# Kernel optimization log

Measured on AMD Instinct MI355X. Metric: run time of the kernel, lower is better.

## Reference

```python
import jax, jax.numpy as jnp
import numpy as np

N = 50000   # nodes
E = 800000  # edges (avg degree 16)
IN = 128    # in_feats
D = 64      # h_feats
H = 4       # n_heads
NEG_SLOPE = 0.2  # DGL GATConv default leaky_relu slope
L = 3       # n_layers (conv_hs)


def setup_inputs() -> dict:
    key = jax.random.key(0)
    ks = jax.random.split(key, 16)
    s = 0.05
    inp = {
        "in_feat": jax.random.normal(ks[0], (N, IN), jnp.float32),
        "src": jax.random.randint(ks[1], (E,), 0, N),
        "dst": jax.random.randint(ks[2], (E,), 0, N),
        # conv1 params (DGL GATConv: fc no bias, attn_l/attn_r, output bias)
        "W1": jax.random.normal(ks[3], (IN, H * D), jnp.float32) * s,
        "al1": jax.random.normal(ks[4], (H, D), jnp.float32) * s,
        "ar1": jax.random.normal(ks[5], (H, D), jnp.float32) * s,
        "b1": jnp.zeros((H * D,), jnp.float32),
        # stacked hidden GATConv params (L layers)
        "Wh": jax.random.normal(ks[6], (L, D, H * D), jnp.float32) * s,
        "alh": jax.random.normal(ks[7], (L, H, D), jnp.float32) * s,
        "arh": jax.random.normal(ks[8], (L, H, D), jnp.float32) * s,
        "bh": jnp.zeros((L, H * D), jnp.float32),
        # out_ln: Linear(H*D -> D)
        "Wo": jax.random.normal(ks[9], (H * D, D), jnp.float32) * s,
        "bo": jnp.zeros((D,), jnp.float32),
    }
    return inp


def gat_conv(h, W, al, ar, b, src, dst):
    # h: [N, F_in] -> feat: [N, H, D]
    feat = (h @ W).reshape(N, H, -1)
    el = jnp.einsum('nhd,hd->nh', feat, al)  # [N, H]
    er = jnp.einsum('nhd,hd->nh', feat, ar)  # [N, H]
    e = jax.nn.leaky_relu(el[src] + er[dst], NEG_SLOPE)  # [E, H]
    # segment softmax over incoming edges of each dst node
    emax = jax.ops.segment_max(e, dst, num_segments=N)
    emax = jnp.where(jnp.isfinite(emax), emax, 0.0)  # guard empty segments
    a = jnp.exp(e - emax[dst])
    ssum = jax.ops.segment_sum(a, dst, num_segments=N)
    alpha = a / ssum[dst]  # [E, H]
    # weighted scatter-aggregate of source features
    out = jax.ops.segment_sum(feat[src] * alpha[:, :, None], dst, num_segments=N)
    return out + b.reshape(1, H, -1)  # [N, H, D]


def reference(in_feat, src, dst, W1, al1, ar1, b1, Wh, alh, arh, bh, Wo, bo):
    h = gat_conv(in_feat, W1, al1, ar1, b1, src, dst).mean(axis=1)  # [N, D]
    for i in range(L - 1):
        h = gat_conv(h, Wh[i], alh[i], arh[i], bh[i], src, dst).mean(axis=1)
    h = gat_conv(h, Wh[L - 1], alh[L - 1], arh[L - 1], bh[L - 1], src, dst)  # [N, H, D]
    h = h.reshape(N, H * D) @ Wo + bo  # [N, D]
    # LayerNorm(elementwise_affine=False)
    mu = h.mean(axis=-1, keepdims=True)
    var = ((h - mu) ** 2).mean(axis=-1, keepdims=True)
    return (h - mu) / jnp.sqrt(var + 1e-5)
```

## Files before the change

### kernel.cpp

```cpp
#include <hip/hip_runtime.h>

#define NN 50000
#define NE 800000

__device__ __forceinline__ float wsum64(float v) {
#pragma unroll
  for (int off = 32; off; off >>= 1) v += __shfl_xor(v, off, 64);
  return v;
}
__device__ __forceinline__ float lrelu(float x) { return x > 0.0f ? x : 0.2f * x; }

__global__ void zero_int_k(int* __restrict__ p, int n) {
  int i = blockIdx.x * 256 + threadIdx.x;
  if (i < n) p[i] = 0;
}

__global__ void count_deg_k(const int* __restrict__ dst, int* __restrict__ deg) {
  int e = blockIdx.x * 256 + threadIdx.x;
  if (e < NE) atomicAdd(&deg[dst[e]], 1);
}

__global__ __launch_bounds__(1024) void scan_k(const int* __restrict__ deg,
                                               int* __restrict__ row_ptr,
                                               int* __restrict__ cursor) {
  __shared__ int woff[16];
  int tid = threadIdx.x;
  int lane = tid & 63, wv = tid >> 6;
  const int CH = (NN + 1023) / 1024;
  int lo = tid * CH;
  int hi = lo + CH;
  if (lo > NN) lo = NN;
  if (hi > NN) hi = NN;
  int s = 0;
  for (int i = lo; i < hi; ++i) s += deg[i];
  int incl = s;
#pragma unroll
  for (int off = 1; off < 64; off <<= 1) {
    int t = __shfl_up(incl, off, 64);
    if (lane >= off) incl += t;
  }
  if (lane == 63) woff[wv] = incl;
  __syncthreads();
  if (tid == 0) {
    int run = 0;
#pragma unroll
    for (int w = 0; w < 16; ++w) { int t = woff[w]; woff[w] = run; run += t; }
    row_ptr[NN] = run;
  }
  __syncthreads();
  int run = incl - s + woff[wv];
  for (int i = lo; i < hi; ++i) {
    row_ptr[i] = run;
    cursor[i] = run;
    run += deg[i];
  }
}

__global__ void fill_csr_k(const int* __restrict__ src, const int* __restrict__ dst,
                           int* __restrict__ cursor, int* __restrict__ csr_src) {
  int e = blockIdx.x * 256 + threadIdx.x;
  if (e < NE) {
    int pos = atomicAdd(&cursor[dst[e]], 1);
    csr_src[pos] = src[e];
  }
}

__global__ void compute_q_k(const float* __restrict__ W, const float* __restrict__ al,
                            const float* __restrict__ ar, float* __restrict__ Q, int KDIM) {
  int idx = blockIdx.x * 256 + threadIdx.x;
  if (idx >= KDIM * 8) return;
  int k = idx >> 3, c = idx & 7;
  int h = c & 3;
  const float* av = (c < 4 ? al : ar) + h * 64;
  const float* wrow = W + (size_t)k * 256 + h * 64;
  float s = 0.0f;
  for (int m = 0; m < 64; ++m) s += wrow[m] * av[m];
  Q[idx] = s;
}

__global__ void compute_m_k(const float* __restrict__ Wh2, const float* __restrict__ Wo,
                            float* __restrict__ M) {
  int row = blockIdx.x;
  int d = threadIdx.x;
  int h = row >> 6, k = row & 63;
  float s = 0.0f;
  for (int j = 0; j < 64; ++j)
    s += Wh2[k * 256 + h * 64 + j] * Wo[(h * 64 + j) * 64 + d];
  M[row * 64 + d] = s;
}

__global__ void compute_c_k(const float* __restrict__ bh2, const float* __restrict__ Wo,
                            const float* __restrict__ bo, float* __restrict__ cvec) {
  int d = threadIdx.x;
  if (d >= 64) return;
  float s = bo[d];
  for (int m = 0; m < 256; ++m) s += bh2[m] * Wo[m * 64 + d];
  cvec[d] = s;
}

__global__ __launch_bounds__(256) void eler_l1_k(const float* __restrict__ X,
                                                 const float* __restrict__ Q,
                                                 float* __restrict__ elp,
                                                 float* __restrict__ erp) {
  int n = __builtin_amdgcn_readfirstlane(blockIdx.x * 4 + (threadIdx.x >> 6));
  int lane = threadIdx.x & 63;
  float2 xv = *(const float2*)&X[(n << 7) + (lane << 1)];
  float4 qa0 = *(const float4*)&Q[(lane * 2) * 8];
  float4 qb0 = *(const float4*)&Q[(lane * 2) * 8 + 4];
  float4 qa1 = *(const float4*)&Q[(lane * 2 + 1) * 8];
  float4 qb1 = *(const float4*)&Q[(lane * 2 + 1) * 8 + 4];
  float p[8];
  p[0] = xv.x * qa0.x + xv.y * qa1.x; p[1] = xv.x * qa0.y + xv.y * qa1.y;
  p[2] = xv.x * qa0.z + xv.y * qa1.z; p[3] = xv.x * qa0.w + xv.y * qa1.w;
  p[4] = xv.x * qb0.x + xv.y * qb1.x; p[5] = xv.x * qb0.y + xv.y * qb1.y;
  p[6] = xv.x * qb0.z + xv.y * qb1.z; p[7] = xv.x * qb0.w + xv.y * qb1.w;
#pragma unroll
  for (int c = 0; c < 8; ++c) p[c] = wsum64(p[c]);
  if (lane == 0) {
    *(float4*)&elp[n << 2] = make_float4(p[0], p[1], p[2], p[3]);
    *(float4*)&erp[n << 2] = make_float4(p[4], p[5], p[6], p[7]);
  }
}

__global__ __launch_bounds__(256) void fused_hidden_k(
    const float* __restrict__ x, const float* __restrict__ el,
    const float* __restrict__ er, const float* __restrict__ W,
    const float* __restrict__ b, const float* __restrict__ Qn,
    const int* __restrict__ row_ptr, const int* __restrict__ csr_src,
    float* __restrict__ hout, float* __restrict__ eln, float* __restrict__ ern) {
  __shared__ float gs[4 * 4 * 256];
  int wave = threadIdx.x >> 6, lane = threadIdx.x & 63;
  int q = lane >> 4, r = lane & 15;
  int base = (blockIdx.x * 4 + wave) * 4;
  float* gw = &gs[wave * 1024];
  int r4 = r << 2;
#pragma unroll 1
  for (int t = 0; t < 4; ++t) {
    int n = __builtin_amdgcn_readfirstlane(base + t);
    int beg = row_ptr[n], end = row_ptr[n + 1];
    float erq = er[(n << 2) + q];
    float4 a = make_float4(0.f, 0.f, 0.f, 0.f);
    float sw = 0.f;
#define ESTEP(elv, xv)                      \
  do {                                      \
    float w = __expf(lrelu((elv) + erq));   \
    sw += w;                                \
    a.x = fmaf(w, (xv).x, a.x);             \
    a.y = fmaf(w, (xv).y, a.y);             \
    a.z = fmaf(w, (xv).z, a.z);             \
    a.w = fmaf(w, (xv).w, a.w);             \
  } while (0)
    int j = beg;
    for (; j + 8 <= end; j += 8) {
      int s0 = csr_src[j + 0], s1 = csr_src[j + 1];
      int s2 = csr_src[j + 2], s3 = csr_src[j + 3];
      int s4 = csr_src[j + 4], s5 = csr_src[j + 5];
      int s6 = csr_src[j + 6], s7 = csr_src[j + 7];
      float e0 = el[(s0 << 2) + q], e1 = el[(s1 << 2) + q];
      float e2 = el[(s2 << 2) + q], e3 = el[(s3 << 2) + q];
      float e4 = el[(s4 << 2) + q], e5 = el[(s5 << 2) + q];
      float e6 = el[(s6 << 2) + q], e7 = el[(s7 << 2) + q];
      float4 x0 = *(const float4*)&x[(s0 << 6) + r4];
      float4 x1 = *(const float4*)&x[(s1 << 6) + r4];
      float4 x2 = *(const float4*)&x[(s2 << 6) + r4];
      float4 x3 = *(const float4*)&x[(s3 << 6) + r4];
      float4 x4 = *(const float4*)&x[(s4 << 6) + r4];
      float4 x5 = *(const float4*)&x[(s5 << 6) + r4];
      float4 x6 = *(const float4*)&x[(s6 << 6) + r4];
      float4 x7 = *(const float4*)&x[(s7 << 6) + r4];
      ESTEP(e0, x0); ESTEP(e1, x1); ESTEP(e2, x2); ESTEP(e3, x3);
      ESTEP(e4, x4); ESTEP(e5, x5); ESTEP(e6, x6); ESTEP(e7, x7);
    }
    for (; j < end; ++j) {
      int s0 = csr_src[j];
      float e0 = el[(s0 << 2) + q];
      float4 x0 = *(const float4*)&x[(s0 << 6) + r4];
      ESTEP(e0, x0);
    }
#undef ESTEP
    float inv = sw > 0.f ? 1.0f / sw : 0.f;
    *(float4*)&gw[t * 256 + (q << 6) + r4] =
        make_float4(a.x * inv, a.y * inv, a.z * inv, a.w * inv);
  }
  float y0 = 0.f, y1 = 0.f, y2 = 0.f, y3 = 0.f;
  for (int rr = 0; rr < 256; rr += 4) {
#pragma unroll
    for (int u = 0; u < 4; ++u) {
      int row = rr + u;
      int h = row >> 6, k = row & 63;
      float sv = W[k * 256 + (h << 6) + lane];
      y0 = fmaf(gw[0 * 256 + row], sv, y0);
      y1 = fmaf(gw[1 * 256 + row], sv, y1);
      y2 = fmaf(gw[2 * 256 + row], sv, y2);
      y3 = fmaf(gw[3 * 256 + row], sv, y3);
    }
  }
  float bsum = b[lane] + b[64 + lane] + b[128 + lane] + b[192 + lane];
  float4 qa = *(const float4*)&Qn[lane * 8];
  float4 qb = *(const float4*)&Qn[lane * 8 + 4];
  float ys[4] = {y0, y1, y2, y3};
#pragma unroll
  for (int t = 0; t < 4; ++t) {
    int n = base + t;
    float yv = 0.25f * (ys[t] + bsum);
    hout[(n << 6) + lane] = yv;
    float e0 = wsum64(yv * qa.x), e1 = wsum64(yv * qa.y);
    float e2 = wsum64(yv * qa.z), e3 = wsum64(yv * qa.w);
    float r0 = wsum64(yv * qb.x), r1 = wsum64(yv * qb.y);
    float r2 = wsum64(yv * qb.z), r3 = wsum64(yv * qb.w);
    if (lane == 0) {
      *(float4*)&eln[n << 2] = make_float4(e0, e1, e2, e3);
      *(float4*)&ern[n << 2] = make_float4(r0, r1, r2, r3);
    }
  }
}

__global__ __launch_bounds__(256) void fused_l1_k(
    const float* __restrict__ x, const float* __restrict__ el,
    const float* __restrict__ er, const float* __restrict__ W,
    const float* __restrict__ b, const float* __restrict__ Qn,
    const int* __restrict__ row_ptr, const int* __restrict__ csr_src,
    float* __restrict__ hout, float* __restrict__ eln, float* __restrict__ ern) {
  __shared__ float gs[4 * 4 * 512];
  int wave = threadIdx.x >> 6, lane = threadIdx.x & 63;
  int q = lane >> 4, r = lane & 15;
  int base = (blockIdx.x * 4 + wave) * 4;
  float* gw = &gs[wave * 2048];
  int r8 = r << 3;
#pragma unroll 1
  for (int t = 0; t < 4; ++t) {
    int n = __builtin_amdgcn_readfirstlane(base + t);
    int beg = row_ptr[n], end = row_ptr[n + 1];
    float erq = er[(n << 2) + q];
    float4 aA = make_float4(0.f, 0.f, 0.f, 0.f);
    float4 aB = make_float4(0.f, 0.f, 0.f, 0.f);
    float sw = 0.f;
#define ESTEP(elv, xa, xb)                  \
  do {                                      \
    float w = __expf(lrelu((elv) + erq));   \
    sw += w;                                \
    aA.x = fmaf(w, (xa).x, aA.x);           \
    aA.y = fmaf(w, (xa).y, aA.y);           \
    aA.z = fmaf(w, (xa).z, aA.z);           \
    aA.w = fmaf(w, (xa).w, aA.w);           \
    aB.x = fmaf(w, (xb).x, aB.x);           \
    aB.y = fmaf(w, (xb).y, aB.y);           \
    aB.z = fmaf(w, (xb).z, aB.z);           \
    aB.w = fmaf(w, (xb).w, aB.w);           \
  } while (0)
    int j = beg;
    for (; j + 4 <= end; j += 4) {
      int s0 = csr_src[j + 0], s1 = csr_src[j + 1];
      int s2 = csr_src[j + 2], s3 = csr_src[j + 3];
      float e0 = el[(s0 << 2) + q], e1 = el[(s1 << 2) + q];
      float e2 = el[(s2 << 2) + q], e3 = el[(s3 << 2) + q];
      float4 xa0 = *(const float4*)&x[(s0 << 7) + r8];
      float4 xb0 = *(const float4*)&x[(s0 << 7) + r8 + 4];
      float4 xa1 = *(const float4*)&x[(s1 << 7) + r8];
      float4 xb1 = *(const float4*)&x[(s1 << 7) + r8 + 4];
      float4 xa2 = *(const float4*)&x[(s2 << 7) + r8];
      float4 xb2 = *(const float4*)&x[(s2 << 7) + r8 + 4];
      float4 xa3 = *(const float4*)&x[(s3 << 7) + r8];
      float4 xb3 = *(const float4*)&x[(s3 << 7) + r8 + 4];
      ESTEP(e0, xa0, xb0); ESTEP(e1, xa1, xb1);
      ESTEP(e2, xa2, xb2); ESTEP(e3, xa3, xb3);
    }
    for (; j < end; ++j) {
      int s0 = csr_src[j];
      float e0 = el[(s0 << 2) + q];
      float4 xa0 = *(const float4*)&x[(s0 << 7) + r8];
      float4 xb0 = *(const float4*)&x[(s0 << 7) + r8 + 4];
      ESTEP(e0, xa0, xb0);
    }
#undef ESTEP
    float inv = sw > 0.f ? 1.0f / sw : 0.f;
    *(float4*)&gw[t * 512 + (q << 7) + r8] =
        make_float4(aA.x * inv, aA.y * inv, aA.z * inv, aA.w * inv);
    *(float4*)&gw[t * 512 + (q << 7) + r8 + 4] =
        make_float4(aB.x * inv, aB.y * inv, aB.z * inv, aB.w * inv);
  }
  float y0 = 0.f, y1 = 0.f, y2 = 0.f, y3 = 0.f;
  for (int rr = 0; rr < 512; rr += 4) {
#pragma unroll
    for (int u = 0; u < 4; ++u) {
      int row = rr + u;
      int h = row >> 7, k = row & 127;
      float sv = W[k * 256 + (h << 6) + lane];
      y0 = fmaf(gw[0 * 512 + row], sv, y0);
      y1 = fmaf(gw[1 * 512 + row], sv, y1);
      y2 = fmaf(gw[2 * 512 + row], sv, y2);
      y3 = fmaf(gw[3 * 512 + row], sv, y3);
    }
  }
  float bsum = b[lane] + b[64 + lane] + b[128 + lane] + b[192 + lane];
  float4 qa = *(const float4*)&Qn[lane * 8];
  float4 qb = *(const float4*)&Qn[lane * 8 + 4];
  float ys[4] = {y0, y1, y2, y3};
#pragma unroll
  for (int t = 0; t < 4; ++t) {
    int n = base + t;
    float yv = 0.25f * (ys[t] + bsum);
    hout[(n << 6) + lane] = yv;
    float e0 = wsum64(yv * qa.x), e1 = wsum64(yv * qa.y);
    float e2 = wsum64(yv * qa.z), e3 = wsum64(yv * qa.w);
    float r0 = wsum64(yv * qb.x), r1 = wsum64(yv * qb.y);
    float r2 = wsum64(yv * qb.z), r3 = wsum64(yv * qb.w);
    if (lane == 0) {
      *(float4*)&eln[n << 2] = make_float4(e0, e1, e2, e3);
      *(float4*)&ern[n << 2] = make_float4(r0, r1, r2, r3);
    }
  }
}

__global__ __launch_bounds__(256) void fused_final_k(
    const float* __restrict__ x, const float* __restrict__ el,
    const float* __restrict__ er, const float* __restrict__ M,
    const float* __restrict__ cvec, const int* __restrict__ row_ptr,
    const int* __restrict__ csr_src, float* __restrict__ out) {
  __shared__ float gs[4 * 4 * 256];
  int wave = threadIdx.x >> 6, lane = threadIdx.x & 63;
  int q = lane >> 4, r = lane & 15;
  int base = (blockIdx.x * 4 + wave) * 4;
  float* gw = &gs[wave * 1024];
  int r4 = r << 2;
#pragma unroll 1
  for (int t = 0; t < 4; ++t) {
    int n = __builtin_amdgcn_readfirstlane(base + t);
    int beg = row_ptr[n], end = row_ptr[n + 1];
    float erq = er[(n << 2) + q];
    float4 a = make_float4(0.f, 0.f, 0.f, 0.f);
    float sw = 0.f;
#define ESTEP(elv, xv)                      \
  do {                                      \
    float w = __expf(lrelu((elv) + erq));   \
    sw += w;                                \
    a.x = fmaf(w, (xv).x, a.x);             \
    a.y = fmaf(w, (xv).y, a.y);             \
    a.z = fmaf(w, (xv).z, a.z);             \
    a.w = fmaf(w, (xv).w, a.w);             \
  } while (0)
    int j = beg;
    for (; j + 8 <= end; j += 8) {
      int s0 = csr_src[j + 0], s1 = csr_src[j + 1];
      int s2 = csr_src[j + 2], s3 = csr_src[j + 3];
      int s4 = csr_src[j + 4], s5 = csr_src[j + 5];
      int s6 = csr_src[j + 6], s7 = csr_src[j + 7];
      float e0 = el[(s0 << 2) + q], e1 = el[(s1 << 2) + q];
      float e2 = el[(s2 << 2) + q], e3 = el[(s3 << 2) + q];
      float e4 = el[(s4 << 2) + q], e5 = el[(s5 << 2) + q];
      float e6 = el[(s6 << 2) + q], e7 = el[(s7 << 2) + q];
      float4 x0 = *(const float4*)&x[(s0 << 6) + r4];
      float4 x1 = *(const float4*)&x[(s1 << 6) + r4];
      float4 x2 = *(const float4*)&x[(s2 << 6) + r4];
      float4 x3 = *(const float4*)&x[(s3 << 6) + r4];
      float4 x4 = *(const float4*)&x[(s4 << 6) + r4];
      float4 x5 = *(const float4*)&x[(s5 << 6) + r4];
      float4 x6 = *(const float4*)&x[(s6 << 6) + r4];
      float4 x7 = *(const float4*)&x[(s7 << 6) + r4];
      ESTEP(e0, x0); ESTEP(e1, x1); ESTEP(e2, x2); ESTEP(e3, x3);
      ESTEP(e4, x4); ESTEP(e5, x5); ESTEP(e6, x6); ESTEP(e7, x7);
    }
    for (; j < end; ++j) {
      int s0 = csr_src[j];
      float e0 = el[(s0 << 2) + q];
      float4 x0 = *(const float4*)&x[(s0 << 6) + r4];
      ESTEP(e0, x0);
    }
#undef ESTEP
    float inv = sw > 0.f ? 1.0f / sw : 0.f;
    *(float4*)&gw[t * 256 + (q << 6) + r4] =
        make_float4(a.x * inv, a.y * inv, a.z * inv, a.w * inv);
  }
  float y0 = 0.f, y1 = 0.f, y2 = 0.f, y3 = 0.f;
  for (int rr = 0; rr < 256; rr += 4) {
#pragma unroll
    for (int u = 0; u < 4; ++u) {
      int row = rr + u;
      float sv = M[(row << 6) + lane];
      y0 = fmaf(gw[0 * 256 + row], sv, y0);
      y1 = fmaf(gw[1 * 256 + row], sv, y1);
      y2 = fmaf(gw[2 * 256 + row], sv, y2);
      y3 = fmaf(gw[3 * 256 + row], sv, y3);
    }
  }
  float cl = cvec[lane];
  float ys[4] = {y0 + cl, y1 + cl, y2 + cl, y3 + cl};
#pragma unroll
  for (int t = 0; t < 4; ++t) {
    int n = base + t;
    float y = ys[t];
    float mu = wsum64(y) * (1.0f / 64.0f);
    float dv = y - mu;
    float var = wsum64(dv * dv) * (1.0f / 64.0f);
    out[(n << 6) + lane] = dv * rsqrtf(var + 1e-5f);
  }
}

extern "C" void kernel_launch(void* const* d_in, const int* in_sizes, int n_in,
                              void* d_out, int out_size, void* d_ws, size_t ws_size,
                              hipStream_t stream) {
  const float* in_feat = (const float*)d_in[0];
  const int* src = (const int*)d_in[1];
  const int* dst = (const int*)d_in[2];
  const float* W1 = (const float*)d_in[3];
  const float* al1 = (const float*)d_in[4];
  const float* ar1 = (const float*)d_in[5];
  const float* b1 = (const float*)d_in[6];
  const float* Wh = (const float*)d_in[7];
  const float* alh = (const float*)d_in[8];
  const float* arh = (const float*)d_in[9];
  const float* bh = (const float*)d_in[10];
  const float* Wo = (const float*)d_in[11];
  const float* bo = (const float*)d_in[12];
  float* out = (float*)d_out;

  char* ws = (char*)d_ws;
  size_t off = 0;
  auto alloc = [&](size_t bytes) {
    void* p = ws + off;
    off = (off + bytes + 255) & ~(size_t)255;
    return p;
  };
  float* h_a = (float*)alloc((size_t)NN * 64 * 4);
  float* h_b = (float*)alloc((size_t)NN * 64 * 4);
  float* el_a = (float*)alloc((size_t)NN * 4 * 4);
  float* er_a = (float*)alloc((size_t)NN * 4 * 4);
  float* el_b = (float*)alloc((size_t)NN * 4 * 4);
  float* er_b = (float*)alloc((size_t)NN * 4 * 4);
  float* Q1 = (float*)alloc(128 * 8 * 4);
  float* Q2 = (float*)alloc(64 * 8 * 4);
  float* Q3 = (float*)alloc(64 * 8 * 4);
  float* Q4 = (float*)alloc(64 * 8 * 4);
  float* M = (float*)alloc(256 * 64 * 4);
  float* cvec = (float*)alloc(64 * 4);
  int* deg = (int*)alloc((size_t)NN * 4);
  int* row_ptr = (int*)alloc((size_t)(NN + 1) * 4);
  int* cursor = (int*)alloc((size_t)NN * 4);
  int* csr_src = (int*)alloc((size_t)NE * 4);
  (void)ws_size; (void)in_sizes; (void)n_in; (void)out_size;

  zero_int_k<<<(NN + 255) / 256, 256, 0, stream>>>(deg, NN);
  count_deg_k<<<(NE + 255) / 256, 256, 0, stream>>>(dst, deg);
  scan_k<<<1, 1024, 0, stream>>>(deg, row_ptr, cursor);
  fill_csr_k<<<(NE + 255) / 256, 256, 0, stream>>>(src, dst, cursor, csr_src);

  compute_q_k<<<4, 256, 0, stream>>>(W1, al1, ar1, Q1, 128);
  compute_q_k<<<2, 256, 0, stream>>>(Wh + 0 * 64 * 256, alh + 0 * 256, arh + 0 * 256, Q2, 64);
  compute_q_k<<<2, 256, 0, stream>>>(Wh + 1 * 64 * 256, alh + 1 * 256, arh + 1 * 256, Q3, 64);
  compute_q_k<<<2, 256, 0, stream>>>(Wh + 2 * 64 * 256, alh + 2 * 256, arh + 2 * 256, Q4, 64);
  compute_m_k<<<256, 64, 0, stream>>>(Wh + 2 * 64 * 256, Wo, M);
  compute_c_k<<<1, 64, 0, stream>>>(bh + 2 * 256, Wo, bo, cvec);

  const int FUSED_GRID = NN / 16;
  const int ELER_GRID = NN / 4;

  eler_l1_k<<<ELER_GRID, 256, 0, stream>>>(in_feat, Q1, el_a, er_a);
  fused_l1_k<<<FUSED_GRID, 256, 0, stream>>>(in_feat, el_a, er_a, W1, b1, Q2,
                                             row_ptr, csr_src, h_a, el_b, er_b);
  fused_hidden_k<<<FUSED_GRID, 256, 0, stream>>>(h_a, el_b, er_b, Wh + 0 * 64 * 256,
                                                 bh + 0 * 256, Q3, row_ptr, csr_src,
                                                 h_b, el_a, er_a);
  fused_hidden_k<<<FUSED_GRID, 256, 0, stream>>>(h_b, el_a, er_a, Wh + 1 * 64 * 256,
                                                 bh + 1 * 256, Q4, row_ptr, csr_src,
                                                 h_a, el_b, er_b);
  fused_final_k<<<FUSED_GRID, 256, 0, stream>>>(h_a, el_b, er_b, M, cvec,
                                                row_ptr, csr_src, out);
}
```

Baseline: 658.3 us.

## Bucket CSR edges by source-node slice to improve gather cache locality

```diff
diff --git a/kernel.cpp b/kernel.cpp
--- a/kernel.cpp
+++ b/kernel.cpp
@@ -2,6 +2,9 @@
 
 #define NN 50000
 #define NE 800000
+#define NB 4
+#define SLICE 12500
+#define NR2 (NN * NB)
 
 __device__ __forceinline__ float wsum64(float v) {
 #pragma unroll
@@ -9,30 +12,35 @@
   return v;
 }
 __device__ __forceinline__ float lrelu(float x) { return x > 0.0f ? x : 0.2f * x; }
+#define RFL(v) __builtin_amdgcn_readfirstlane(v)
 
 __global__ void zero_int_k(int* __restrict__ p, int n) {
   int i = blockIdx.x * 256 + threadIdx.x;
   if (i < n) p[i] = 0;
 }
 
-__global__ void count_deg_k(const int* __restrict__ dst, int* __restrict__ deg) {
+__global__ void count_deg2_k(const int* __restrict__ src, const int* __restrict__ dst,
+                             int* __restrict__ deg2) {
   int e = blockIdx.x * 256 + threadIdx.x;
-  if (e < NE) atomicAdd(&deg[dst[e]], 1);
-}
-
-__global__ __launch_bounds__(1024) void scan_k(const int* __restrict__ deg,
-                                               int* __restrict__ row_ptr,
-                                               int* __restrict__ cursor) {
+  if (e < NE) {
+    int b = src[e] / SLICE;
+    atomicAdd(&deg2[dst[e] * NB + b], 1);
+  }
+}
+
+__global__ __launch_bounds__(1024) void scan2_k(const int* __restrict__ deg2,
+                                                int* __restrict__ rp2,
+                                                int* __restrict__ cur2) {
   __shared__ int woff[16];
   int tid = threadIdx.x;
   int lane = tid & 63, wv = tid >> 6;
-  const int CH = (NN + 1023) / 1024;
+  const int CH = (NR2 + 1023) / 1024;
   int lo = tid * CH;
   int hi = lo + CH;
-  if (lo > NN) lo = NN;
-  if (hi > NN) hi = NN;
+  if (lo > NR2) lo = NR2;
+  if (hi > NR2) hi = NR2;
   int s = 0;
-  for (int i = lo; i < hi; ++i) s += deg[i];
+  for (int i = lo; i < hi; ++i) s += deg2[i];
   int incl = s;
 #pragma unroll
   for (int off = 1; off < 64; off <<= 1) {
@@ -45,23 +53,25 @@
     int run = 0;
 #pragma unroll
     for (int w = 0; w < 16; ++w) { int t = woff[w]; woff[w] = run; run += t; }
-    row_ptr[NN] = run;
+    rp2[NR2] = run;
   }
   __syncthreads();
   int run = incl - s + woff[wv];
   for (int i = lo; i < hi; ++i) {
-    row_ptr[i] = run;
-    cursor[i] = run;
-    run += deg[i];
-  }
-}
-
-__global__ void fill_csr_k(const int* __restrict__ src, const int* __restrict__ dst,
-                           int* __restrict__ cursor, int* __restrict__ csr_src) {
+    rp2[i] = run;
+    cur2[i] = run;
+    run += deg2[i];
+  }
+}
+
+__global__ void fill_csr2_k(const int* __restrict__ src, const int* __restrict__ dst,
+                            int* __restrict__ cur2, int* __restrict__ csr_src) {
   int e = blockIdx.x * 256 + threadIdx.x;
   if (e < NE) {
-    int pos = atomicAdd(&cursor[dst[e]], 1);
-    csr_src[pos] = src[e];
+    int sv = src[e];
+    int b = sv / SLICE;
+    int pos = atomicAdd(&cur2[dst[e] * NB + b], 1);
+    csr_src[pos] = sv;
   }
 }
 
@@ -102,7 +112,7 @@
                                                  const float* __restrict__ Q,
                                                  float* __restrict__ elp,
                                                  float* __restrict__ erp) {
-  int n = __builtin_amdgcn_readfirstlane(blockIdx.x * 4 + (threadIdx.x >> 6));
+  int n = RFL(blockIdx.x * 4 + (threadIdx.x >> 6));
   int lane = threadIdx.x & 63;
   float2 xv = *(const float2*)&X[(n << 7) + (lane << 1)];
   float4 qa0 = *(const float4*)&Q[(lane * 2) * 8];
@@ -122,65 +132,129 @@
   }
 }
 
+__device__ __forceinline__ void agg_bucket64(const float* __restrict__ x,
+                                             const float* __restrict__ el,
+                                             const int* __restrict__ csr,
+                                             int beg, int end, int q, int r4,
+                                             float erq, float4& a, float& sw) {
+  int j = beg;
+  for (; j + 4 <= end; j += 4) {
+    int s0 = csr[j + 0], s1 = csr[j + 1], s2 = csr[j + 2], s3 = csr[j + 3];
+    float e0 = el[(s0 << 2) + q], e1 = el[(s1 << 2) + q];
+    float e2 = el[(s2 << 2) + q], e3 = el[(s3 << 2) + q];
+    float4 x0 = *(const float4*)&x[(s0 << 6) + r4];
+    float4 x1 = *(const float4*)&x[(s1 << 6) + r4];
+    float4 x2 = *(const float4*)&x[(s2 << 6) + r4];
+    float4 x3 = *(const float4*)&x[(s3 << 6) + r4];
+    float w0 = __expf(lrelu(e0 + erq)), w1 = __expf(lrelu(e1 + erq));
+    float w2 = __expf(lrelu(e2 + erq)), w3 = __expf(lrelu(e3 + erq));
+    sw += w0 + w1 + w2 + w3;
+    a.x = fmaf(w0, x0.x, a.x); a.y = fmaf(w0, x0.y, a.y);
+    a.z = fmaf(w0, x0.z, a.z); a.w = fmaf(w0, x0.w, a.w);
+    a.x = fmaf(w1, x1.x, a.x); a.y = fmaf(w1, x1.y, a.y);
+    a.z = fmaf(w1, x1.z, a.z); a.w = fmaf(w1, x1.w, a.w);
+    a.x = fmaf(w2, x2.x, a.x); a.y = fmaf(w2, x2.y, a.y);
+    a.z = fmaf(w2, x2.z, a.z); a.w = fmaf(w2, x2.w, a.w);
+    a.x = fmaf(w3, x3.x, a.x); a.y = fmaf(w3, x3.y, a.y);
+    a.z = fmaf(w3, x3.z, a.z); a.w = fmaf(w3, x3.w, a.w);
+  }
+  for (; j < end; ++j) {
+    int s0 = csr[j];
+    float e0 = el[(s0 << 2) + q];
+    float4 x0 = *(const float4*)&x[(s0 << 6) + r4];
+    float w0 = __expf(lrelu(e0 + erq));
+    sw += w0;
+    a.x = fmaf(w0, x0.x, a.x); a.y = fmaf(w0, x0.y, a.y);
+    a.z = fmaf(w0, x0.z, a.z); a.w = fmaf(w0, x0.w, a.w);
+  }
+}
+
+__device__ __forceinline__ void agg_bucket128(const float* __restrict__ x,
+                                              const float* __restrict__ el,
+                                              const int* __restrict__ csr,
+                                              int beg, int end, int q, int r8,
+                                              float erq, float4& aA, float4& aB,
+                                              float& sw) {
+  int j = beg;
+  for (; j + 4 <= end; j += 4) {
+    int s0 = csr[j + 0], s1 = csr[j + 1], s2 = csr[j + 2], s3 = csr[j + 3];
+    float e0 = el[(s0 << 2) + q], e1 = el[(s1 << 2) + q];
+    float e2 = el[(s2 << 2) + q], e3 = el[(s3 << 2) + q];
+    float4 xa0 = *(const float4*)&x[(s0 << 7) + r8];
+    float4 xb0 = *(const float4*)&x[(s0 << 7) + r8 + 4];
+    float4 xa1 = *(const float4*)&x[(s1 << 7) + r8];
+    float4 xb1 = *(const float4*)&x[(s1 << 7) + r8 + 4];
+    float4 xa2 = *(const float4*)&x[(s2 << 7) + r8];
+    float4 xb2 = *(const float4*)&x[(s2 << 7) + r8 + 4];
+    float4 xa3 = *(const float4*)&x[(s3 << 7) + r8];
+    float4 xb3 = *(const float4*)&x[(s3 << 7) + r8 + 4];
+    float w0 = __expf(lrelu(e0 + erq)), w1 = __expf(lrelu(e1 + erq));
+    float w2 = __expf(lrelu(e2 + erq)), w3 = __expf(lrelu(e3 + erq));
+    sw += w0 + w1 + w2 + w3;
+    aA.x = fmaf(w0, xa0.x, aA.x); aA.y = fmaf(w0, xa0.y, aA.y);
+    aA.z = fmaf(w0, xa0.z, aA.z); aA.w = fmaf(w0, xa0.w, aA.w);
+    aB.x = fmaf(w0, xb0.x, aB.x); aB.y = fmaf(w0, xb0.y, aB.y);
+    aB.z = fmaf(w0, xb0.z, aB.z); aB.w = fmaf(w0, xb0.w, aB.w);
+    aA.x = fmaf(w1, xa1.x, aA.x); aA.y = fmaf(w1, xa1.y, aA.y);
+    aA.z = fmaf(w1, xa1.z, aA.z); aA.w = fmaf(w1, xa1.w, aA.w);
+    aB.x = fmaf(w1, xb1.x, aB.x); aB.y = fmaf(w1, xb1.y, aB.y);
+    aB.z = fmaf(w1, xb1.z, aB.z); aB.w = fmaf(w1, xb1.w, aB.w);
+    aA.x = fmaf(w2, xa2.x, aA.x); aA.y = fmaf(w2, xa2.y, aA.y);
+    aA.z = fmaf(w2, xa2.z, aA.z); aA.w = fmaf(w2, xa2.w, aA.w);
+    aB.x = fmaf(w2, xb2.x, aB.x); aB.y = fmaf(w2, xb2.y, aB.y);
+    aB.z = fmaf(w2, xb2.z, aB.z); aB.w = fmaf(w2, xb2.w, aB.w);
+    aA.x = fmaf(w3, xa3.x, aA.x); aA.y = fmaf(w3, xa3.y, aA.y);
+    aA.z = fmaf(w3, xa3.z, aA.z); aA.w = fmaf(w3, xa3.w, aA.w);
+    aB.x = fmaf(w3, xb3.x, aB.x); aB.y = fmaf(w3, xb3.y, aB.y);
+    aB.z = fmaf(w3, xb3.z, aB.z); aB.w = fmaf(w3, xb3.w, aB.w);
+  }
+  for (; j < end; ++j) {
+    int s0 = csr[j];
+    float e0 = el[(s0 << 2) + q];
+    float4 xa0 = *(const float4*)&x[(s0 << 7) + r8];
+    float4 xb0 = *(const float4*)&x[(s0 << 7) + r8 + 4];
+    float w0 = __expf(lrelu(e0 + erq));
+    sw += w0;
+    aA.x = fmaf(w0, xa0.x, aA.x); aA.y = fmaf(w0, xa0.y, aA.y);
+    aA.z = fmaf(w0, xa0.z, aA.z); aA.w = fmaf(w0, xa0.w, aA.w);
+    aB.x = fmaf(w0, xb0.x, aB.x); aB.y = fmaf(w0, xb0.y, aB.y);
+    aB.z = fmaf(w0, xb0.z, aB.z); aB.w = fmaf(w0, xb0.w, aB.w);
+  }
+}
+
 __global__ __launch_bounds__(256) void fused_hidden_k(
     const float* __restrict__ x, const float* __restrict__ el,
     const float* __restrict__ er, const float* __restrict__ W,
     const float* __restrict__ b, const float* __restrict__ Qn,
-    const int* __restrict__ row_ptr, const int* __restrict__ csr_src,
+    const int* __restrict__ rp2, const int* __restrict__ csr_src,
     float* __restrict__ hout, float* __restrict__ eln, float* __restrict__ ern) {
-  __shared__ float gs[4 * 4 * 256];
+  __shared__ float gs[4][1024];
   int wave = threadIdx.x >> 6, lane = threadIdx.x & 63;
-  int q = lane >> 4, r = lane & 15;
+  int q = lane >> 4, r = lane & 15, r4 = r << 2;
   int base = (blockIdx.x * 4 + wave) * 4;
-  float* gw = &gs[wave * 1024];
-  int r4 = r << 2;
+  float* gw = gs[wave];
+  float4 av[4];
+  float swv[4], erqv[4];
+#pragma unroll
+  for (int t = 0; t < 4; ++t) {
+    av[t] = make_float4(0.f, 0.f, 0.f, 0.f);
+    swv[t] = 0.f;
+    erqv[t] = er[((base + t) << 2) + q];
+  }
 #pragma unroll 1
-  for (int t = 0; t < 4; ++t) {
-    int n = __builtin_amdgcn_readfirstlane(base + t);
-    int beg = row_ptr[n], end = row_ptr[n + 1];
-    float erq = er[(n << 2) + q];
-    float4 a = make_float4(0.f, 0.f, 0.f, 0.f);
-    float sw = 0.f;
-#define ESTEP(elv, xv)                      \
-  do {                                      \
-    float w = __expf(lrelu((elv) + erq));   \
-    sw += w;                                \
-    a.x = fmaf(w, (xv).x, a.x);             \
-    a.y = fmaf(w, (xv).y, a.y);             \
-    a.z = fmaf(w, (xv).z, a.z);             \
-    a.w = fmaf(w, (xv).w, a.w);             \
-  } while (0)
-    int j = beg;
-    for (; j + 8 <= end; j += 8) {
-      int s0 = csr_src[j + 0], s1 = csr_src[j + 1];
-      int s2 = csr_src[j + 2], s3 = csr_src[j + 3];
-      int s4 = csr_src[j + 4], s5 = csr_src[j + 5];
-      int s6 = csr_src[j + 6], s7 = csr_src[j + 7];
-      float e0 = el[(s0 << 2) + q], e1 = el[(s1 << 2) + q];
-      float e2 = el[(s2 << 2) + q], e3 = el[(s3 << 2) + q];
-      float e4 = el[(s4 << 2) + q], e5 = el[(s5 << 2) + q];
-      float e6 = el[(s6 << 2) + q], e7 = el[(s7 << 2) + q];
-      float4 x0 = *(const float4*)&x[(s0 << 6) + r4];
-      float4 x1 = *(const float4*)&x[(s1 << 6) + r4];
-      float4 x2 = *(const float4*)&x[(s2 << 6) + r4];
-      float4 x3 = *(const float4*)&x[(s3 << 6) + r4];
-      float4 x4 = *(const float4*)&x[(s4 << 6) + r4];
-      float4 x5 = *(const float4*)&x[(s5 << 6) + r4];
-      float4 x6 = *(const float4*)&x[(s6 << 6) + r4];
-      float4 x7 = *(const float4*)&x[(s7 << 6) + r4];
-      ESTEP(e0, x0); ESTEP(e1, x1); ESTEP(e2, x2); ESTEP(e3, x3);
-      ESTEP(e4, x4); ESTEP(e5, x5); ESTEP(e6, x6); ESTEP(e7, x7);
-    }
-    for (; j < end; ++j) {
-      int s0 = csr_src[j];
-      float e0 = el[(s0 << 2) + q];
-      float4 x0 = *(const float4*)&x[(s0 << 6) + r4];
-      ESTEP(e0, x0);
-    }
-#undef ESTEP
-    float inv = sw > 0.f ? 1.0f / sw : 0.f;
+  for (int bkt = 0; bkt < NB; ++bkt) {
+#pragma unroll
+    for (int t = 0; t < 4; ++t) {
+      int nb = RFL((base + t) * NB + bkt);
+      int beg = rp2[nb], end = rp2[nb + 1];
+      agg_bucket64(x, el, csr_src, beg, end, q, r4, erqv[t], av[t], swv[t]);
+    }
+  }
+#pragma unroll
+  for (int t = 0; t < 4; ++t) {
+    float inv = swv[t] > 0.f ? 1.0f / swv[t] : 0.f;
     *(float4*)&gw[t * 256 + (q << 6) + r4] =
-        make_float4(a.x * inv, a.y * inv, a.z * inv, a.w * inv);
+        make_float4(av[t].x * inv, av[t].y * inv, av[t].z * inv, av[t].w * inv);
   }
   float y0 = 0.f, y1 = 0.f, y2 = 0.f, y3 = 0.f;
   for (int rr = 0; rr < 256; rr += 4) {
@@ -219,65 +293,38 @@
     const float* __restrict__ x, const float* __restrict__ el,
     const float* __restrict__ er, const float* __restrict__ W,
     const float* __restrict__ b, const float* __restrict__ Qn,
-    const int* __restrict__ row_ptr, const int* __restrict__ csr_src,
+    const int* __restrict__ rp2, const int* __restrict__ csr_src,
     float* __restrict__ hout, float* __restrict__ eln, float* __restrict__ ern) {
-  __shared__ float gs[4 * 4 * 512];
+  __shared__ float gs[4][2048];
   int wave = threadIdx.x >> 6, lane = threadIdx.x & 63;
-  int q = lane >> 4, r = lane & 15;
+  int q = lane >> 4, r = lane & 15, r8 = r << 3;
   int base = (blockIdx.x * 4 + wave) * 4;
-  float* gw = &gs[wave * 2048];
-  int r8 = r << 3;
+  float* gw = gs[wave];
+  float4 aAv[4], aBv[4];
+  float swv[4], erqv[4];
+#pragma unroll
+  for (int t = 0; t < 4; ++t) {
+    aAv[t] = make_float4(0.f, 0.f, 0.f, 0.f);
+    aBv[t] = make_float4(0.f, 0.f, 0.f, 0.f);
+    swv[t] = 0.f;
+    erqv[t] = er[((base + t) << 2) + q];
+  }
 #pragma unroll 1
-  for (int t = 0; t < 4; ++t) {
-    int n = __builtin_amdgcn_readfirstlane(base + t);
-    int beg = row_ptr[n], end = row_ptr[n + 1];
-    float erq = er[(n << 2) + q];
-    float4 aA = make_float4(0.f, 0.f, 0.f, 0.f);
-    float4 aB = make_float4(0.f, 0.f, 0.f, 0.f);
-    float sw = 0.f;
-#define ESTEP(elv, xa, xb)                  \
-  do {                                      \
-    float w = __expf(lrelu((elv) + erq));   \
-    sw += w;                                \
-    aA.x = fmaf(w, (xa).x, aA.x);           \
-    aA.y = fmaf(w, (xa).y, aA.y);           \
-    aA.z = fmaf(w, (xa).z, aA.z);           \
-    aA.w = fmaf(w, (xa).w, aA.w);           \
-    aB.x = fmaf(w, (xb).x, aB.x);           \
-    aB.y = fmaf(w, (xb).y, aB.y);           \
-    aB.z = fmaf(w, (xb).z, aB.z);           \
-    aB.w = fmaf(w, (xb).w, aB.w);           \
-  } while (0)
-    int j = beg;
-    for (; j + 4 <= end; j += 4) {
-      int s0 = csr_src[j + 0], s1 = csr_src[j + 1];
-      int s2 = csr_src[j + 2], s3 = csr_src[j + 3];
-      float e0 = el[(s0 << 2) + q], e1 = el[(s1 << 2) + q];
-      float e2 = el[(s2 << 2) + q], e3 = el[(s3 << 2) + q];
-      float4 xa0 = *(const float4*)&x[(s0 << 7) + r8];
-      float4 xb0 = *(const float4*)&x[(s0 << 7) + r8 + 4];
-      float4 xa1 = *(const float4*)&x[(s1 << 7) + r8];
-      float4 xb1 = *(const float4*)&x[(s1 << 7) + r8 + 4];
-      float4 xa2 = *(const float4*)&x[(s2 << 7) + r8];
-      float4 xb2 = *(const float4*)&x[(s2 << 7) + r8 + 4];
-      float4 xa3 = *(const float4*)&x[(s3 << 7) + r8];
-      float4 xb3 = *(const float4*)&x[(s3 << 7) + r8 + 4];
-      ESTEP(e0, xa0, xb0); ESTEP(e1, xa1, xb1);
-      ESTEP(e2, xa2, xb2); ESTEP(e3, xa3, xb3);
-    }
-    for (; j < end; ++j) {
-      int s0 = csr_src[j];
-      float e0 = el[(s0 << 2) + q];
-      float4 xa0 = *(const float4*)&x[(s0 << 7) + r8];
-      float4 xb0 = *(const float4*)&x[(s0 << 7) + r8 + 4];
-      ESTEP(e0, xa0, xb0);
-    }
-#undef ESTEP
-    float inv = sw > 0.f ? 1.0f / sw : 0.f;
+  for (int bkt = 0; bkt < NB; ++bkt) {
+#pragma unroll
+    for (int t = 0; t < 4; ++t) {
+      int nb = RFL((base + t) * NB + bkt);
+      int beg = rp2[nb], end = rp2[nb + 1];
+      agg_bucket128(x, el, csr_src, beg, end, q, r8, erqv[t], aAv[t], aBv[t], swv[t]);
+    }
+  }
+#pragma unroll
+  for (int t = 0; t < 4; ++t) {
+    float inv = swv[t] > 0.f ? 1.0f / swv[t] : 0.f;
     *(float4*)&gw[t * 512 + (q << 7) + r8] =
-        make_float4(aA.x * inv, aA.y * inv, aA.z * inv, aA.w * inv);
+        make_float4(aAv[t].x * inv, aAv[t].y * inv, aAv[t].z * inv, aAv[t].w * inv);
     *(float4*)&gw[t * 512 + (q << 7) + r8 + 4] =
-        make_float4(aB.x * inv, aB.y * inv, aB.z * inv, aB.w * inv);
+        make_float4(aBv[t].x * inv, aBv[t].y * inv, aBv[t].z * inv, aBv[t].w * inv);
   }
   float y0 = 0.f, y1 = 0.f, y2 = 0.f, y3 = 0.f;
   for (int rr = 0; rr < 512; rr += 4) {
@@ -315,61 +362,35 @@
 __global__ __launch_bounds__(256) void fused_final_k(
     const float* __restrict__ x, const float* __restrict__ el,
     const float* __restrict__ er, const float* __restrict__ M,
-    const float* __restrict__ cvec, const int* __restrict__ row_ptr,
+    const float* __restrict__ cvec, const int* __restrict__ rp2,
     const int* __restrict__ csr_src, float* __restrict__ out) {
-  __shared__ float gs[4 * 4 * 256];
+  __shared__ float gs[4][1024];
   int wave = threadIdx.x >> 6, lane = threadIdx.x & 63;
-  int q = lane >> 4, r = lane & 15;
+  int q = lane >> 4, r = lane & 15, r4 = r << 2;
   int base = (blockIdx.x * 4 + wave) * 4;
-  float* gw = &gs[wave * 1024];
-  int r4 = r << 2;
+  float* gw = gs[wave];
+  float4 av[4];
+  float swv[4], erqv[4];
+#pragma unroll
+  for (int t = 0; t < 4; ++t) {
+    av[t] = make_float4(0.f, 0.f, 0.f, 0.f);
+    swv[t] = 0.f;
+    erqv[t] = er[((base + t) << 2) + q];
+  }
 #pragma unroll 1
-  for (int t = 0; t < 4; ++t) {
-    int n = __builtin_amdgcn_readfirstlane(base + t);
-    int beg = row_ptr[n], end = row_ptr[n + 1];
-    float erq = er[(n << 2) + q];
-    float4 a = make_float4(0.f, 0.f, 0.f, 0.f);
-    float sw = 0.f;
-#define ESTEP(elv, xv)                      \
-  do {                                      \
-    float w = __expf(lrelu((elv) + erq));   \
-    sw += w;                                \
-    a.x = fmaf(w, (xv).x, a.x);             \
-    a.y = fmaf(w, (xv).y, a.y);             \
-    a.z = fmaf(w, (xv).z, a.z);             \
-    a.w = fmaf(w, (xv).w, a.w);             \
-  } while (0)
-    int j = beg;
-    for (; j + 8 <= end; j += 8) {
-      int s0 = csr_src[j + 0], s1 = csr_src[j + 1];
-      int s2 = csr_src[j + 2], s3 = csr_src[j + 3];
-      int s4 = csr_src[j + 4], s5 = csr_src[j + 5];
-      int s6 = csr_src[j + 6], s7 = csr_src[j + 7];
-      float e0 = el[(s0 << 2) + q], e1 = el[(s1 << 2) + q];
-      float e2 = el[(s2 << 2) + q], e3 = el[(s3 << 2) + q];
-      float e4 = el[(s4 << 2) + q], e5 = el[(s5 << 2) + q];
-      float e6 = el[(s6 << 2) + q], e7 = el[(s7 << 2) + q];
-      float4 x0 = *(const float4*)&x[(s0 << 6) + r4];
-      float4 x1 = *(const float4*)&x[(s1 << 6) + r4];
-      float4 x2 = *(const float4*)&x[(s2 << 6) + r4];
-      float4 x3 = *(const float4*)&x[(s3 << 6) + r4];
-      float4 x4 = *(const float4*)&x[(s4 << 6) + r4];
-      float4 x5 = *(const float4*)&x[(s5 << 6) + r4];
-      float4 x6 = *(const float4*)&x[(s6 << 6) + r4];
-      float4 x7 = *(const float4*)&x[(s7 << 6) + r4];
-      ESTEP(e0, x0); ESTEP(e1, x1); ESTEP(e2, x2); ESTEP(e3, x3);
-      ESTEP(e4, x4); ESTEP(e5, x5); ESTEP(e6, x6); ESTEP(e7, x7);
-    }
-    for (; j < end; ++j) {
-      int s0 = csr_src[j];
-      float e0 = el[(s0 << 2) + q];
-      float4 x0 = *(const float4*)&x[(s0 << 6) + r4];
-      ESTEP(e0, x0);
-    }
-#undef ESTEP
-    float inv = sw > 0.f ? 1.0f / sw : 0.f;
+  for (int bkt = 0; bkt < NB; ++bkt) {
+#pragma unroll
+    for (int t = 0; t < 4; ++t) {
+      int nb = RFL((base + t) * NB + bkt);
+      int beg = rp2[nb], end = rp2[nb + 1];
+      agg_bucket64(x, el, csr_src, beg, end, q, r4, erqv[t], av[t], swv[t]);
+    }
+  }
+#pragma unroll
+  for (int t = 0; t < 4; ++t) {
+    float inv = swv[t] > 0.f ? 1.0f / swv[t] : 0.f;
     *(float4*)&gw[t * 256 + (q << 6) + r4] =
-        make_float4(a.x * inv, a.y * inv, a.z * inv, a.w * inv);
+        make_float4(av[t].x * inv, av[t].y * inv, av[t].z * inv, av[t].w * inv);
   }
   float y0 = 0.f, y1 = 0.f, y2 = 0.f, y3 = 0.f;
   for (int rr = 0; rr < 256; rr += 4) {
@@ -433,16 +454,16 @@
   float* Q4 = (float*)alloc(64 * 8 * 4);
   float* M = (float*)alloc(256 * 64 * 4);
   float* cvec = (float*)alloc(64 * 4);
-  int* deg = (int*)alloc((size_t)NN * 4);
-  int* row_ptr = (int*)alloc((size_t)(NN + 1) * 4);
-  int* cursor = (int*)alloc((size_t)NN * 4);
+  int* deg2 = (int*)alloc((size_t)NR2 * 4);
+  int* rp2 = (int*)alloc((size_t)(NR2 + 1) * 4);
+  int* cur2 = (int*)alloc((size_t)NR2 * 4);
   int* csr_src = (int*)alloc((size_t)NE * 4);
   (void)ws_size; (void)in_sizes; (void)n_in; (void)out_size;
 
-  zero_int_k<<<(NN + 255) / 256, 256, 0, stream>>>(deg, NN);
-  count_deg_k<<<(NE + 255) / 256, 256, 0, stream>>>(dst, deg);
-  scan_k<<<1, 1024, 0, stream>>>(deg, row_ptr, cursor);
-  fill_csr_k<<<(NE + 255) / 256, 256, 0, stream>>>(src, dst, cursor, csr_src);
+  zero_int_k<<<(NR2 + 255) / 256, 256, 0, stream>>>(deg2, NR2);
+  count_deg2_k<<<(NE + 255) / 256, 256, 0, stream>>>(src, dst, deg2);
+  scan2_k<<<1, 1024, 0, stream>>>(deg2, rp2, cur2);
+  fill_csr2_k<<<(NE + 255) / 256, 256, 0, stream>>>(src, dst, cur2, csr_src);
 
   compute_q_k<<<4, 256, 0, stream>>>(W1, al1, ar1, Q1, 128);
   compute_q_k<<<2, 256, 0, stream>>>(Wh + 0 * 64 * 256, alh + 0 * 256, arh + 0 * 256, Q2, 64);
@@ -456,13 +477,13 @@
 
   eler_l1_k<<<ELER_GRID, 256, 0, stream>>>(in_feat, Q1, el_a, er_a);
   fused_l1_k<<<FUSED_GRID, 256, 0, stream>>>(in_feat, el_a, er_a, W1, b1, Q2,
-                                             row_ptr, csr_src, h_a, el_b, er_b);
+                                             rp2, csr_src, h_a, el_b, er_b);
   fused_hidden_k<<<FUSED_GRID, 256, 0, stream>>>(h_a, el_b, er_b, Wh + 0 * 64 * 256,
-                                                 bh + 0 * 256, Q3, row_ptr, csr_src,
+                                                 bh + 0 * 256, Q3, rp2, csr_src,
                                                  h_b, el_a, er_a);
   fused_hidden_k<<<FUSED_GRID, 256, 0, stream>>>(h_b, el_a, er_a, Wh + 1 * 64 * 256,
-                                                 bh + 1 * 256, Q4, row_ptr, csr_src,
+                                                 bh + 1 * 256, Q4, rp2, csr_src,
                                                  h_a, el_b, er_b);
   fused_final_k<<<FUSED_GRID, 256, 0, stream>>>(h_a, el_b, er_b, M, cvec,
-                                                row_ptr, csr_src, out);
-}
+                                                rp2, csr_src, out);
+}
```

Result: slower. 1.020 ms (+54.9%).
